# Optimization experiments

Hardware: AMD Instinct MI355X
Metric: run time of the kernel (lower is better)

The kernel has to match this reference:

```python
import jax, jax.numpy as jnp
import numpy as np

OBS_DIM, GOAL_DIM, NUM_SKILLS, ACTION_DIM = 256, 64, 16, 32
HIDDEN = 128
BATCH = 65536


def setup_inputs() -> dict:
    key = jax.random.key(0)
    ks = jax.random.split(key, 10)
    s = lambda k, shape, fan_in: jax.random.normal(k, shape, jnp.float32) * (1.0 / np.sqrt(fan_in))
    return {
        "obs": jax.random.normal(ks[0], (BATCH, OBS_DIM), jnp.float32),
        "goals": jax.random.normal(ks[1], (BATCH, GOAL_DIM), jnp.float32),
        # gate (AlphaNet) params
        "Wa1": s(ks[2], (OBS_DIM + GOAL_DIM, HIDDEN), OBS_DIM + GOAL_DIM),
        "ba1": jnp.zeros((HIDDEN,), jnp.float32),
        "Wa2": s(ks[3], (HIDDEN, NUM_SKILLS), HIDDEN),
        "ba2": jnp.zeros((NUM_SKILLS,), jnp.float32),
        # stacked executor params: [S, in, out]
        "W1": s(ks[4], (NUM_SKILLS, OBS_DIM, HIDDEN), OBS_DIM),
        "b1": jnp.zeros((NUM_SKILLS, HIDDEN), jnp.float32),
        "W2": s(ks[5], (NUM_SKILLS, HIDDEN, ACTION_DIM), HIDDEN),
        "b2": jnp.zeros((NUM_SKILLS, ACTION_DIM), jnp.float32),
    }


def reference(obs, goals, Wa1, ba1, Wa2, ba2, W1, b1, W2, b2):
    # gate: softmax(Linear(ReLU(Linear(cat(obs, goals)))))
    concat_input = jnp.concatenate([obs, goals], axis=-1)  # [B, O+G]
    ha = jax.nn.relu(concat_input @ Wa1 + ba1)             # [B, H]
    alphas = jax.nn.softmax(ha @ Wa2 + ba2, axis=-1)       # [B, S]

    # all experts as one grouped GEMM over stacked weights
    h = jax.nn.relu(jnp.einsum("bo,soh->bsh", obs, W1) + b1[None])  # [B, S, H]
    skill_outputs = jnp.einsum("bsh,sha->bsa", h, W2) + b2[None]    # [B, S, A]

    # weighted sum over skills
    mixed_action = jnp.einsum("bsa,bs->ba", skill_outputs, alphas)  # [B, A]
    return mixed_action, alphas
```

## Files before the change

kernel.cpp:

```cpp
#include <hip/hip_runtime.h>


typedef __attribute__((ext_vector_type(8))) short    bf16x8;
typedef __attribute__((ext_vector_type(4))) float    f32x4;
typedef __attribute__((ext_vector_type(4))) _Float16 f16x4;
using half2v = decltype(__builtin_amdgcn_cvt_pkrtz(0.f, 0.f));

#define GATE_W1_OFF   0
#define GATE_W2_OFF   81920
#define GATE_BA1_OFF  86016
#define GATE_BA2_OFF  86528
#define GATE_BYTES    86592
#define S_W1_STRIDE   528
#define S_W2_OFF      67584
#define S_W2_STRIDE   272
#define S_B1_OFF      76288
#define S_B2_OFF      76800
#define S_IMG         76928
#define LDS_BYTES     163520

__device__ __forceinline__ unsigned short f2bf(float f) {
  unsigned u = __builtin_bit_cast(unsigned, f);
  return (unsigned short)((u + 0x7FFFu + ((u >> 16) & 1u)) >> 16);
}

__device__ __forceinline__ bf16x8 pack_bf8(f32x4 a, f32x4 b) {
  int4 r;
  asm("v_cvt_pk_bf16_f32 %0, %1, %2" : "=v"(r.x) : "v"(a[0]), "v"(a[1]));
  asm("v_cvt_pk_bf16_f32 %0, %1, %2" : "=v"(r.y) : "v"(a[2]), "v"(a[3]));
  asm("v_cvt_pk_bf16_f32 %0, %1, %2" : "=v"(r.z) : "v"(b[0]), "v"(b[1]));
  asm("v_cvt_pk_bf16_f32 %0, %1, %2" : "=v"(r.w) : "v"(b[2]), "v"(b[3]));
  return __builtin_bit_cast(bf16x8, r);
}

#define RELU_SCALE_PACK(dst, v, av, z)                                   \
  {                                                                      \
    half2v lo_ = __builtin_amdgcn_cvt_pkrtz((v)[0], (v)[1]);             \
    half2v hi_ = __builtin_amdgcn_cvt_pkrtz((v)[2], (v)[3]);             \
    lo_ = __builtin_elementwise_max(lo_, z) * (av);                      \
    hi_ = __builtin_elementwise_max(hi_, z) * (av);                      \
    dst[0] = (_Float16)lo_[0]; dst[1] = (_Float16)lo_[1];                \
    dst[2] = (_Float16)hi_[0]; dst[3] = (_Float16)hi_[1];                \
  }
#define RELU_PACK(dst, v, z)                                             \
  {                                                                      \
    half2v lo_ = __builtin_amdgcn_cvt_pkrtz((v)[0], (v)[1]);             \
    half2v hi_ = __builtin_amdgcn_cvt_pkrtz((v)[2], (v)[3]);             \
    lo_ = __builtin_elementwise_max(lo_, z);                             \
    hi_ = __builtin_elementwise_max(hi_, z);                             \
    dst[0] = (_Float16)lo_[0]; dst[1] = (_Float16)lo_[1];                \
    dst[2] = (_Float16)hi_[0]; dst[3] = (_Float16)hi_[1];                \
  }

__global__ void prep_weights(const float* __restrict__ Wa1, const float* __restrict__ Wa2,
                             const float* __restrict__ ba1, const float* __restrict__ ba2,
                             const float* __restrict__ W1,  const float* __restrict__ W2,
                             const float* __restrict__ b1,  const float* __restrict__ b2,
                             unsigned char* __restrict__ ws) {
  int i = blockIdx.x * 256 + threadIdx.x;
  if (i < 524288) {
    int s = i >> 15, r = i & 32767, h = r >> 8, o = r & 255;
    float v = W1[(s * 256 + o) * 128 + h];
    *(unsigned short*)(ws + GATE_BYTES + s * S_IMG + h * S_W1_STRIDE + 2 * o) = f2bf(v);
  } else if (i < 589824) {
    int j = i - 524288, s = j >> 12, r = j & 4095, a = r >> 7, h = r & 127;
    float v = W2[(s * 128 + h) * 32 + a];
    *(_Float16*)(ws + GATE_BYTES + s * S_IMG + S_W2_OFF + a * S_W2_STRIDE + 2 * h) =
        (_Float16)v;
  } else if (i < 630784) {
    int j = i - 589824, h = j / 320, o = j - h * 320;
    float v = Wa1[o * 128 + h];
    *(unsigned short*)(ws + GATE_W1_OFF + h * 640 +
                       ((2 * o) ^ ((h & 7) << 4))) = f2bf(v);
  } else if (i < 632832) {
    int j = i - 630784, n = j >> 7, h = j & 127;
    float v = Wa2[h * 16 + n];
    *(_Float16*)(ws + GATE_W2_OFF + n * 256 +
                 ((2 * h) ^ ((n & 7) << 3))) = (_Float16)v;
  } else if (i < 634880) {
    int j = i - 632832, s = j >> 7, h = j & 127;
    *(float*)(ws + GATE_BYTES + s * S_IMG + S_B1_OFF + 4 * h) = b1[s * 128 + h];
  } else if (i < 635392) {
    int j = i - 634880, s = j >> 5, a = j & 31;
    *(float*)(ws + GATE_BYTES + s * S_IMG + S_B2_OFF + 4 * a) = b2[s * 32 + a];
  } else if (i < 635520) {
    int j = i - 635392;
    *(float*)(ws + GATE_BA1_OFF + 4 * j) = ba1[j];
  } else if (i < 635536) {
    int j = i - 635520;
    *(float*)(ws + GATE_BA2_OFF + 4 * j) = ba2[j];
  }
}

__device__ __forceinline__ void stage_lin(const unsigned char* gsrc, unsigned char* ldst,
                                          int tid, int bytes) {
  for (int off = tid * 16; off < bytes; off += 512 * 16) {
    __builtin_amdgcn_global_load_lds(
        (const __attribute__((address_space(1))) unsigned int*)(const void*)(gsrc + off),
        (__attribute__((address_space(3))) unsigned int*)(void*)(ldst + off), 16, 0, 0);
  }
}

__global__ __launch_bounds__(512, 2)
void mop_fused(const float* __restrict__ obs, const float* __restrict__ goals,
               const unsigned char* __restrict__ ws, float* __restrict__ dout) {
  extern __shared__ unsigned char smem[];
  const int tid  = threadIdx.x;
  const int lane = tid & 63;
  const int wave = tid >> 6;
  const int half = wave >> 2;
  const int pr   = wave & 3;
  const int l15  = lane & 15;
  const int g    = lane >> 4;
  const int swz4 = (lane & 7) << 4;
  const int swz3 = (lane & 7) << 3;
  const int rowbase = blockIdx.x * 256 + pr * 64;

  float* out_mixed = dout;
  float* out_alpha = dout + 65536 * 32;

  const int lw1 = half * 33792 + l15 * S_W1_STRIDE + 16 * g;
  const int lw2 = S_W2_OFF + l15 * S_W2_STRIDE + 8 * g + half * 128;
  const int lb1 = S_B1_OFF + 256 * half + 16 * g;
  const int lb2 = S_B2_OFF + 16 * g;

  stage_lin(ws, smem, tid, GATE_BYTES);

  bf16x8 obsf[4][8];
  #pragma unroll
  for (int nb = 0; nb < 4; ++nb) {
    const float* rp = obs + (size_t)(rowbase + nb * 16 + l15) * 256 + 8 * g;
    #pragma unroll
    for (int t = 0; t < 8; ++t) {
      f32x4 a = *(const f32x4*)(rp + 32 * t);
      f32x4 c = *(const f32x4*)(rp + 32 * t + 4);
      obsf[nb][t] = pack_bf8(a, c);
    }
  }

  const half2v zh = __builtin_amdgcn_cvt_pkrtz(0.f, 0.f);
  f32x4 lacc[4];
  {
    bf16x8 goalf[4][2];
    #pragma unroll
    for (int nb = 0; nb < 4; ++nb) {
      const float* gp = goals + (size_t)(rowbase + nb * 16 + l15) * 64 + 8 * g;
      #pragma unroll
      for (int t = 0; t < 2; ++t) {
        f32x4 a = *(const f32x4*)(gp + 32 * t);
        f32x4 c = *(const f32x4*)(gp + 32 * t + 4);
        goalf[nb][t] = pack_bf8(a, c);
      }
    }

    __syncthreads();
    stage_lin(ws + GATE_BYTES, smem + GATE_BYTES, tid, S_IMG);

    #pragma unroll
    for (int p = 0; p < 2; ++p) {
      f32x4 gacc[2][4];
      #pragma unroll
      for (int ht = 0; ht < 4; ++ht) {
        f32x4 bias = *(const f32x4*)(smem + GATE_BA1_OFF + 256 * half + 64 * ht + 16 * g);
        gacc[0][ht] = bias; gacc[1][ht] = bias;
      }
      #pragma unroll
      for (int t = 0; t < 10; ++t) {
        bf16x8 bf0 = (t < 8) ? obsf[2 * p][t]     : goalf[2 * p][t - 8];
        bf16x8 bf1 = (t < 8) ? obsf[2 * p + 1][t] : goalf[2 * p + 1][t - 8];
        #pragma unroll
        for (int ht = 0; ht < 4; ++ht) {
          int row = 64 * half + 16 * ht + l15;
          bf16x8 af = *(const bf16x8*)(smem + GATE_W1_OFF + row * 640 +
                                       ((64 * t + 16 * g) ^ swz4));
          gacc[0][ht] = __builtin_amdgcn_mfma_f32_16x16x32_bf16(af, bf0, gacc[0][ht], 0, 0, 0);
          gacc[1][ht] = __builtin_amdgcn_mfma_f32_16x16x32_bf16(af, bf1, gacc[1][ht], 0, 0, 0);
        }
      }
      #pragma unroll
      for (int j = 0; j < 2; ++j) {
        const int nb = 2 * p + j;
        lacc[nb] = (half == 0) ? *(const f32x4*)(smem + GATE_BA2_OFF + 16 * g)
                               : f32x4{0.f, 0.f, 0.f, 0.f};
        #pragma unroll
        for (int ht = 0; ht < 4; ++ht) {
          f16x4 hf;
          RELU_PACK(hf, gacc[j][ht], zh);
          f16x4 wf = *(const f16x4*)(smem + GATE_W2_OFF + l15 * 256 +
                                     ((32 * (4 * half + ht) + 8 * g) ^ swz3));
          lacc[nb] = __builtin_amdgcn_mfma_f32_16x16x16f16(wf, hf, lacc[nb], 0, 0, 0);
        }
      }
    }
  }

  __syncthreads();
  #pragma unroll
  for (int nb = 0; nb < 4; ++nb)
    #pragma unroll
    for (int r = 0; r < 4; ++r)
      *(float*)(smem + wave * 4352 + nb * 1088 + (4 * g + r) * 68 + 4 * l15) = lacc[nb][r];
  __syncthreads();

  half2v alph_pk[4][2];
  #pragma unroll
  for (int nb = 0; nb < 4; ++nb) {
    f32x4 l = lacc[nb];
    #pragma unroll
    for (int r = 0; r < 4; ++r)
      l[r] += *(const float*)(smem + (wave ^ 4) * 4352 + nb * 1088 + (4 * g + r) * 68 + 4 * l15);
    float m = fmaxf(fmaxf(l[0], l[1]), fmaxf(l[2], l[3]));
    m = fmaxf(m, __shfl_xor(m, 16, 64));
    m = fmaxf(m, __shfl_xor(m, 32, 64));
    f32x4 e;
    e[0] = __expf(l[0] - m); e[1] = __expf(l[1] - m);
    e[2] = __expf(l[2] - m); e[3] = __expf(l[3] - m);
    float ssum = e[0] + e[1] + e[2] + e[3];
    ssum += __shfl_xor(ssum, 16, 64);
    ssum += __shfl_xor(ssum, 32, 64);
    f32x4 al = e * (1.0f / ssum);
    if (half == 0)
      *(f32x4*)(out_alpha + (size_t)(rowbase + nb * 16 + l15) * 16 + 4 * g) = al;
    alph_pk[nb][0] = __builtin_amdgcn_cvt_pkrtz(al[0], al[1]);
    alph_pk[nb][1] = __builtin_amdgcn_cvt_pkrtz(al[2], al[3]);
  }

  __syncthreads();

  f32x4 macc[4][2] = {};
  for (int s = 0; s < 16; ++s) {
    const unsigned char* buf = smem + ((s & 1) ? 0 : GATE_BYTES);
    if (s < 15) {
      unsigned char* nbuf = smem + (((s + 1) & 1) ? 0 : GATE_BYTES);
      stage_lin(ws + GATE_BYTES + (size_t)(s + 1) * S_IMG, nbuf, tid, S_IMG);
    }
    const int asrc = ((s >> 2) << 4) | l15;
    float av[4];
    half2v ah[4];
    #pragma unroll
    for (int nb = 0; nb < 4; ++nb) {
      float pkf = __builtin_bit_cast(float, alph_pk[nb][(s >> 1) & 1]);
      half2v th = __builtin_bit_cast(half2v, __shfl(pkf, asrc, 64));
      auto sel = (s & 1) ? th[1] : th[0];
      half2v a2; a2[0] = sel; a2[1] = sel;
      ah[nb] = a2;
      av[nb] = (float)sel;
    }

    const unsigned char* w1p = buf + lw1;
    const unsigned char* w2p = buf + lw2;

    __builtin_amdgcn_s_setprio(1);
    #pragma unroll
    for (int ht = 0; ht < 4; ++ht) {
      f32x4 b1v = *(const f32x4*)(buf + lb1 + 64 * ht);
      f32x4 acc[4];
      #pragma unroll
      for (int nb = 0; nb < 4; ++nb) acc[nb] = b1v;
      #pragma unroll
      for (int t = 0; t < 8; ++t) {
        bf16x8 af = *(const bf16x8*)(w1p + ht * 8448 + t * 64);
        #pragma unroll
        for (int nb = 0; nb < 4; ++nb)
          acc[nb] = __builtin_amdgcn_mfma_f32_16x16x32_bf16(af, obsf[nb][t], acc[nb], 0, 0, 0);
      }
      f16x4 hf[4];
      #pragma unroll
      for (int nb = 0; nb < 4; ++nb) RELU_SCALE_PACK(hf[nb], acc[nb], ah[nb], zh);
      #pragma unroll
      for (int ta = 0; ta < 2; ++ta) {
        f16x4 wf = *(const f16x4*)(w2p + ta * 4352 + ht * 32);
        #pragma unroll
        for (int nb = 0; nb < 4; ++nb)
          macc[nb][ta] = __builtin_amdgcn_mfma_f32_16x16x16f16(wf, hf[nb], macc[nb][ta], 0, 0, 0);
      }
    }
    __builtin_amdgcn_s_setprio(0);
    if (half == 0) {
      #pragma unroll
      for (int ta = 0; ta < 2; ++ta) {
        f32x4 b2v = *(const f32x4*)(buf + lb2 + 64 * ta);
        #pragma unroll
        for (int nb = 0; nb < 4; ++nb)
          macc[nb][ta] = macc[nb][ta] + b2v * av[nb];
      }
    }
    __syncthreads();
  }

  #pragma unroll
  for (int nb = 0; nb < 4; ++nb)
    #pragma unroll
    for (int ta = 0; ta < 2; ++ta)
      #pragma unroll
      for (int r = 0; r < 4; ++r)
        *(float*)(smem + wave * 8704 + nb * 2176 + (16 * ta + 4 * g + r) * 68 + 4 * l15) =
            macc[nb][ta][r];
  __syncthreads();
  #pragma unroll
  for (int j = 0; j < 2; ++j) {
    const int nb = 2 * half + j;
    #pragma unroll
    for (int ta = 0; ta < 2; ++ta) {
      f32x4 v = macc[nb][ta];
      #pragma unroll
      for (int r = 0; r < 4; ++r)
        v[r] += *(const float*)(smem + (wave ^ 4) * 8704 + nb * 2176 +
                                (16 * ta + 4 * g + r) * 68 + 4 * l15);
      *(f32x4*)(out_mixed + (size_t)(rowbase + nb * 16 + l15) * 32 + 16 * ta + 4 * g) = v;
    }
  }
}

extern "C" void kernel_launch(void* const* d_in, const int* in_sizes, int n_in,
                              void* d_out, int out_size, void* d_ws, size_t ws_size,
                              hipStream_t stream) {
  const float* obs   = (const float*)d_in[0];
  const float* goals = (const float*)d_in[1];
  const float* Wa1   = (const float*)d_in[2];
  const float* ba1   = (const float*)d_in[3];
  const float* Wa2   = (const float*)d_in[4];
  const float* ba2   = (const float*)d_in[5];
  const float* W1    = (const float*)d_in[6];
  const float* b1    = (const float*)d_in[7];
  const float* W2    = (const float*)d_in[8];
  const float* b2    = (const float*)d_in[9];
  unsigned char* ws  = (unsigned char*)d_ws;
  float* out = (float*)d_out;

  prep_weights<<<2483, 256, 0, stream>>>(Wa1, Wa2, ba1, ba2, W1, W2, b1, b2, ws);
  mop_fused<<<256, 512, LDS_BYTES, stream>>>(obs, goals, ws, out);
}
```

Baseline: 108.9 us.

## Double block to 1024 threads with 32 rows per wave and LDS alpha table

Each block now runs 16 waves instead of 8, and each wave handles 32 rows instead of 64. This halves per-wave register arrays (obs fragments, accumulators) and doubles the waves resident per CU for latency hiding. Alpha values are broadcast through a small fp16 table in LDS instead of per-step cross-lane shuffles. In exchange, each weight fragment read from LDS feeds only two MFMAs instead of four, so LDS read traffic per unit of work roughly doubles.

```diff
diff --git a/kernel.cpp b/kernel.cpp
--- a/kernel.cpp
+++ b/kernel.cpp
@@ -17,6 +17,7 @@
 #define S_B1_OFF      76288
 #define S_B2_OFF      76800
 #define S_IMG         76928
+#define ALPHA_TBL     76928
 #define LDS_BYTES     163520
 
 __device__ __forceinline__ unsigned short f2bf(float f) {
@@ -94,27 +95,27 @@
 
 __device__ __forceinline__ void stage_lin(const unsigned char* gsrc, unsigned char* ldst,
                                           int tid, int bytes) {
-  for (int off = tid * 16; off < bytes; off += 512 * 16) {
+  for (int off = tid * 16; off < bytes; off += 1024 * 16) {
     __builtin_amdgcn_global_load_lds(
         (const __attribute__((address_space(1))) unsigned int*)(const void*)(gsrc + off),
         (__attribute__((address_space(3))) unsigned int*)(void*)(ldst + off), 16, 0, 0);
   }
 }
 
-__global__ __launch_bounds__(512, 2)
+__global__ __launch_bounds__(1024, 4)
 void mop_fused(const float* __restrict__ obs, const float* __restrict__ goals,
                const unsigned char* __restrict__ ws, float* __restrict__ dout) {
   extern __shared__ unsigned char smem[];
   const int tid  = threadIdx.x;
   const int lane = tid & 63;
   const int wave = tid >> 6;
-  const int half = wave >> 2;
-  const int pr   = wave & 3;
+  const int half = wave >> 3;
+  const int pr   = wave & 7;
   const int l15  = lane & 15;
   const int g    = lane >> 4;
   const int swz4 = (lane & 7) << 4;
   const int swz3 = (lane & 7) << 3;
-  const int rowbase = blockIdx.x * 256 + pr * 64;
+  const int rowbase = blockIdx.x * 256 + pr * 32;
 
   float* out_mixed = dout;
   float* out_alpha = dout + 65536 * 32;
@@ -126,9 +127,9 @@
 
   stage_lin(ws, smem, tid, GATE_BYTES);
 
-  bf16x8 obsf[4][8];
+  bf16x8 obsf[2][8];
   #pragma unroll
-  for (int nb = 0; nb < 4; ++nb) {
+  for (int nb = 0; nb < 2; ++nb) {
     const float* rp = obs + (size_t)(rowbase + nb * 16 + l15) * 256 + 8 * g;
     #pragma unroll
     for (int t = 0; t < 8; ++t) {
@@ -139,11 +140,11 @@
   }
 
   const half2v zh = __builtin_amdgcn_cvt_pkrtz(0.f, 0.f);
-  f32x4 lacc[4];
+  f32x4 lacc[2];
   {
-    bf16x8 goalf[4][2];
-    #pragma unroll
-    for (int nb = 0; nb < 4; ++nb) {
+    bf16x8 goalf[2][2];
+    #pragma unroll
+    for (int nb = 0; nb < 2; ++nb) {
       const float* gp = goals + (size_t)(rowbase + nb * 16 + l15) * 64 + 8 * g;
       #pragma unroll
       for (int t = 0; t < 2; ++t) {
@@ -157,37 +158,43 @@
     stage_lin(ws + GATE_BYTES, smem + GATE_BYTES, tid, S_IMG);
 
     #pragma unroll
-    for (int p = 0; p < 2; ++p) {
-      f32x4 gacc[2][4];
-      #pragma unroll
-      for (int ht = 0; ht < 4; ++ht) {
-        f32x4 bias = *(const f32x4*)(smem + GATE_BA1_OFF + 256 * half + 64 * ht + 16 * g);
-        gacc[0][ht] = bias; gacc[1][ht] = bias;
+    for (int nb = 0; nb < 2; ++nb)
+      lacc[nb] = (half == 0) ? *(const f32x4*)(smem + GATE_BA2_OFF + 16 * g)
+                             : f32x4{0.f, 0.f, 0.f, 0.f};
+
+    #pragma unroll
+    for (int hp = 0; hp < 2; ++hp) {
+      f32x4 gacc[2][2];
+      #pragma unroll
+      for (int hl = 0; hl < 2; ++hl) {
+        f32x4 bias = *(const f32x4*)(smem + GATE_BA1_OFF + 256 * half +
+                                     64 * (2 * hp + hl) + 16 * g);
+        gacc[0][hl] = bias; gacc[1][hl] = bias;
       }
       #pragma unroll
       for (int t = 0; t < 10; ++t) {
-        bf16x8 bf0 = (t < 8) ? obsf[2 * p][t]     : goalf[2 * p][t - 8];
-        bf16x8 bf1 = (t < 8) ? obsf[2 * p + 1][t] : goalf[2 * p + 1][t - 8];
         #pragma unroll
-        for (int ht = 0; ht < 4; ++ht) {
-          int row = 64 * half + 16 * ht + l15;
+        for (int hl = 0; hl < 2; ++hl) {
+          int row = 64 * half + 16 * (2 * hp + hl) + l15;
           bf16x8 af = *(const bf16x8*)(smem + GATE_W1_OFF + row * 640 +
                                        ((64 * t + 16 * g) ^ swz4));
-          gacc[0][ht] = __builtin_amdgcn_mfma_f32_16x16x32_bf16(af, bf0, gacc[0][ht], 0, 0, 0);
-          gacc[1][ht] = __builtin_amdgcn_mfma_f32_16x16x32_bf16(af, bf1, gacc[1][ht], 0, 0, 0);
+          if (t < 8) {
+            gacc[0][hl] = __builtin_amdgcn_mfma_f32_16x16x32_bf16(af, obsf[0][t], gacc[0][hl], 0, 0, 0);
+            gacc[1][hl] = __builtin_amdgcn_mfma_f32_16x16x32_bf16(af, obsf[1][t], gacc[1][hl], 0, 0, 0);
+          } else {
+            gacc[0][hl] = __builtin_amdgcn_mfma_f32_16x16x32_bf16(af, goalf[0][t - 8], gacc[0][hl], 0, 0, 0);
+            gacc[1][hl] = __builtin_amdgcn_mfma_f32_16x16x32_bf16(af, goalf[1][t - 8], gacc[1][hl], 0, 0, 0);
+          }
         }
       }
       #pragma unroll
-      for (int j = 0; j < 2; ++j) {
-        const int nb = 2 * p + j;
-        lacc[nb] = (half == 0) ? *(const f32x4*)(smem + GATE_BA2_OFF + 16 * g)
-                               : f32x4{0.f, 0.f, 0.f, 0.f};
+      for (int nb = 0; nb < 2; ++nb) {
         #pragma unroll
-        for (int ht = 0; ht < 4; ++ht) {
+        for (int hl = 0; hl < 2; ++hl) {
           f16x4 hf;
-          RELU_PACK(hf, gacc[j][ht], zh);
+          RELU_PACK(hf, gacc[nb][hl], zh);
           f16x4 wf = *(const f16x4*)(smem + GATE_W2_OFF + l15 * 256 +
-                                     ((32 * (4 * half + ht) + 8 * g) ^ swz3));
+                                     ((32 * (4 * half + 2 * hp + hl) + 8 * g) ^ swz3));
           lacc[nb] = __builtin_amdgcn_mfma_f32_16x16x16f16(wf, hf, lacc[nb], 0, 0, 0);
         }
       }
@@ -196,19 +203,18 @@
 
   __syncthreads();
   #pragma unroll
-  for (int nb = 0; nb < 4; ++nb)
+  for (int nb = 0; nb < 2; ++nb)
     #pragma unroll
     for (int r = 0; r < 4; ++r)
-      *(float*)(smem + wave * 4352 + nb * 1088 + (4 * g + r) * 68 + 4 * l15) = lacc[nb][r];
+      *(float*)(smem + wave * 2176 + nb * 1088 + (4 * g + r) * 68 + 4 * l15) = lacc[nb][r];
   __syncthreads();
 
-  half2v alph_pk[4][2];
   #pragma unroll
-  for (int nb = 0; nb < 4; ++nb) {
+  for (int nb = 0; nb < 2; ++nb) {
     f32x4 l = lacc[nb];
     #pragma unroll
     for (int r = 0; r < 4; ++r)
-      l[r] += *(const float*)(smem + (wave ^ 4) * 4352 + nb * 1088 + (4 * g + r) * 68 + 4 * l15);
+      l[r] += *(const float*)(smem + (wave ^ 8) * 2176 + nb * 1088 + (4 * g + r) * 68 + 4 * l15);
     float m = fmaxf(fmaxf(l[0], l[1]), fmaxf(l[2], l[3]));
     m = fmaxf(m, __shfl_xor(m, 16, 64));
     m = fmaxf(m, __shfl_xor(m, 32, 64));
@@ -219,32 +225,32 @@
     ssum += __shfl_xor(ssum, 16, 64);
     ssum += __shfl_xor(ssum, 32, 64);
     f32x4 al = e * (1.0f / ssum);
-    if (half == 0)
+    if (half == 0) {
       *(f32x4*)(out_alpha + (size_t)(rowbase + nb * 16 + l15) * 16 + 4 * g) = al;
-    alph_pk[nb][0] = __builtin_amdgcn_cvt_pkrtz(al[0], al[1]);
-    alph_pk[nb][1] = __builtin_amdgcn_cvt_pkrtz(al[2], al[3]);
+      #pragma unroll
+      for (int r = 0; r < 4; ++r)
+        *(_Float16*)(smem + ALPHA_TBL + (4 * g + r) * 544 +
+                     (pr * 32 + nb * 16 + l15) * 2) = (_Float16)al[r];
+    }
   }
 
   __syncthreads();
 
-  f32x4 macc[4][2] = {};
+  f32x4 macc[2][2] = {};
   for (int s = 0; s < 16; ++s) {
     const unsigned char* buf = smem + ((s & 1) ? 0 : GATE_BYTES);
     if (s < 15) {
       unsigned char* nbuf = smem + (((s + 1) & 1) ? 0 : GATE_BYTES);
       stage_lin(ws + GATE_BYTES + (size_t)(s + 1) * S_IMG, nbuf, tid, S_IMG);
     }
-    const int asrc = ((s >> 2) << 4) | l15;
-    float av[4];
-    half2v ah[4];
-    #pragma unroll
-    for (int nb = 0; nb < 4; ++nb) {
-      float pkf = __builtin_bit_cast(float, alph_pk[nb][(s >> 1) & 1]);
-      half2v th = __builtin_bit_cast(half2v, __shfl(pkf, asrc, 64));
-      auto sel = (s & 1) ? th[1] : th[0];
-      half2v a2; a2[0] = sel; a2[1] = sel;
+    half2v ah[2];
+    #pragma unroll
+    for (int nb = 0; nb < 2; ++nb) {
+      unsigned short raw = *(const unsigned short*)(
+          smem + ALPHA_TBL + s * 544 + (pr * 32 + nb * 16 + l15) * 2);
+      __fp16 hv = __builtin_bit_cast(__fp16, raw);
+      half2v a2; a2[0] = hv; a2[1] = hv;
       ah[nb] = a2;
-      av[nb] = (float)sel;
     }
 
     const unsigned char* w1p = buf + lw1;
@@ -254,58 +260,55 @@
     #pragma unroll
     for (int ht = 0; ht < 4; ++ht) {
       f32x4 b1v = *(const f32x4*)(buf + lb1 + 64 * ht);
-      f32x4 acc[4];
-      #pragma unroll
-      for (int nb = 0; nb < 4; ++nb) acc[nb] = b1v;
+      f32x4 acc0 = b1v, acc1 = b1v;
       #pragma unroll
       for (int t = 0; t < 8; ++t) {
         bf16x8 af = *(const bf16x8*)(w1p + ht * 8448 + t * 64);
-        #pragma unroll
-        for (int nb = 0; nb < 4; ++nb)
-          acc[nb] = __builtin_amdgcn_mfma_f32_16x16x32_bf16(af, obsf[nb][t], acc[nb], 0, 0, 0);
-      }
-      f16x4 hf[4];
-      #pragma unroll
-      for (int nb = 0; nb < 4; ++nb) RELU_SCALE_PACK(hf[nb], acc[nb], ah[nb], zh);
+        acc0 = __builtin_amdgcn_mfma_f32_16x16x32_bf16(af, obsf[0][t], acc0, 0, 0, 0);
+        acc1 = __builtin_amdgcn_mfma_f32_16x16x32_bf16(af, obsf[1][t], acc1, 0, 0, 0);
+      }
+      f16x4 hf0, hf1;
+      RELU_SCALE_PACK(hf0, acc0, ah[0], zh);
+      RELU_SCALE_PACK(hf1, acc1, ah[1], zh);
       #pragma unroll
       for (int ta = 0; ta < 2; ++ta) {
         f16x4 wf = *(const f16x4*)(w2p + ta * 4352 + ht * 32);
-        #pragma unroll
-        for (int nb = 0; nb < 4; ++nb)
-          macc[nb][ta] = __builtin_amdgcn_mfma_f32_16x16x16f16(wf, hf[nb], macc[nb][ta], 0, 0, 0);
+        macc[0][ta] = __builtin_amdgcn_mfma_f32_16x16x16f16(wf, hf0, macc[0][ta], 0, 0, 0);
+        macc[1][ta] = __builtin_amdgcn_mfma_f32_16x16x16f16(wf, hf1, macc[1][ta], 0, 0, 0);
       }
     }
     __builtin_amdgcn_s_setprio(0);
     if (half == 0) {
       #pragma unroll
-      for (int ta = 0; ta < 2; ++ta) {
-        f32x4 b2v = *(const f32x4*)(buf + lb2 + 64 * ta);
+      for (int nb = 0; nb < 2; ++nb) {
+        float av = (float)ah[nb][0];
         #pragma unroll
-        for (int nb = 0; nb < 4; ++nb)
-          macc[nb][ta] = macc[nb][ta] + b2v * av[nb];
+        for (int ta = 0; ta < 2; ++ta) {
+          f32x4 b2v = *(const f32x4*)(buf + lb2 + 64 * ta);
+          macc[nb][ta] = macc[nb][ta] + b2v * av;
+        }
       }
     }
     __syncthreads();
   }
 
   #pragma unroll
-  for (int nb = 0; nb < 4; ++nb)
+  for (int nb = 0; nb < 2; ++nb)
     #pragma unroll
     for (int ta = 0; ta < 2; ++ta)
       #pragma unroll
       for (int r = 0; r < 4; ++r)
-        *(float*)(smem + wave * 8704 + nb * 2176 + (16 * ta + 4 * g + r) * 68 + 4 * l15) =
+        *(float*)(smem + wave * 4352 + nb * 2176 + (16 * ta + 4 * g + r) * 68 + 4 * l15) =
             macc[nb][ta][r];
   __syncthreads();
-  #pragma unroll
-  for (int j = 0; j < 2; ++j) {
-    const int nb = 2 * half + j;
+  {
+    const int nb = half;
     #pragma unroll
     for (int ta = 0; ta < 2; ++ta) {
       f32x4 v = macc[nb][ta];
       #pragma unroll
       for (int r = 0; r < 4; ++r)
-        v[r] += *(const float*)(smem + (wave ^ 4) * 8704 + nb * 2176 +
+        v[r] += *(const float*)(smem + (wave ^ 8) * 4352 + nb * 2176 +
                                 (16 * ta + 4 * g + r) * 68 + 4 * l15);
       *(f32x4*)(out_mixed + (size_t)(rowbase + nb * 16 + l15) * 32 + 16 * ta + 4 * g) = v;
     }
@@ -329,5 +332,5 @@
   float* out = (float*)d_out;
 
   prep_weights<<<2483, 256, 0, stream>>>(Wa1, Wa2, ba1, ba2, W1, W2, b1, b2, ws);
-  mop_fused<<<256, 512, LDS_BYTES, stream>>>(obs, goals, ws, out);
-}
+  mop_fused<<<256, 1024, LDS_BYTES, stream>>>(obs, goals, ws, out);
+}
```

Measured after the change: 108.8 us. About the same (-0.1%).
